# Optimization experiments

Hardware: AMD Instinct MI355X
Metric: run time of the kernel (lower is better)

## Reference

```python
import jax, jax.numpy as jnp
import numpy as np

EMB = 1024
HEADS = 16
HEAD_DIM = EMB // HEADS


def setup_inputs() -> dict:
    key = jax.random.key(0)
    ks = jax.random.split(key, 6)
    B, S = 4, 1024
    inputs = jax.random.normal(ks[0], (B, S, EMB), dtype=jnp.float32)
    # causal mask: 1.0 where attention is disallowed (added * -1e9 in the layer)
    mask = (1.0 - jnp.tril(jnp.ones((S, S), dtype=jnp.float32)))[None, None, :, :]
    scale = 1.0 / np.sqrt(EMB)
    wq = jax.random.normal(ks[1], (EMB, EMB), dtype=jnp.float32) * scale
    wk = jax.random.normal(ks[2], (EMB, EMB), dtype=jnp.float32) * scale
    wv = jax.random.normal(ks[3], (EMB, EMB), dtype=jnp.float32) * scale
    wo = jax.random.normal(ks[4], (EMB, EMB), dtype=jnp.float32) * scale
    zb = jnp.zeros((EMB,), dtype=jnp.float32)
    return {"inputs": inputs, "mask": mask, "wq": wq, "bq": zb, "wk": wk,
            "bk": zb, "wv": wv, "bv": zb, "wo": wo, "bo": zb}


def _split_heads(t, B):
    # [B, S, E] -> [B, H, S, Dh]
    return t.reshape(B, -1, HEADS, HEAD_DIM).transpose(0, 2, 1, 3)


def reference(inputs, mask, wq, bq, wk, bk, wv, bv, wo, bo):
    B = inputs.shape[0]
    q = _split_heads(inputs @ wq + bq, B)
    k = _split_heads(inputs @ wk + bk, B)
    v = _split_heads(inputs @ wv + bv, B)
    # NOTE: source divides by sqrt(sqrt(head_num)) = head_num**0.25
    scores = jnp.einsum('bhsd,bhtd->bhst', q, k) / jnp.asarray(HEADS, inputs.dtype) ** 0.25
    if mask is not None:
        scores = scores + mask * -1e9
    attn = jax.nn.softmax(scores, axis=-1)
    z = jnp.einsum('bhst,bhtd->bhsd', attn, v)
    # Faithful to source: reshape [B,H,S,Dh] -> [B,S,E] WITHOUT transposing heads back
    z = z.reshape(B, -1, EMB)
    return z @ wo + bo
```

## Files before the change

### kernel.cpp

```cpp
#include <hip/hip_runtime.h>
#include <hip/hip_bf16.h>
#include <stdint.h>

typedef __attribute__((ext_vector_type(8))) short short8;
typedef __attribute__((ext_vector_type(4))) float float4v;

#define SEQ   1024
#define NQKV  3072

__device__ __forceinline__ float bf2f(ushort h) {
    union { uint u; float f; } c; c.u = ((uint)h) << 16; return c.f;
}
__device__ __forceinline__ ushort f2bf(float f) {
    union { uint u; float f; } c; c.f = f;
    uint u = c.u;
    return (ushort)((u + 0x7fffu + ((u >> 16) & 1u)) >> 16);
}
__device__ __forceinline__ void gl2lds16(const ushort* g, ushort* l) {
    __builtin_amdgcn_global_load_lds(
        (const __attribute__((address_space(1))) unsigned int*)(g),
        (__attribute__((address_space(3))) unsigned int*)(l),
        16, 0, 0);
}

__global__ __launch_bounds__(256) void prep_k(const void* __restrict__ X,
                                              const void* __restrict__ w0,
                                              const void* __restrict__ w1,
                                              const void* __restrict__ w2,
                                              const void* __restrict__ w3,
                                              const void* __restrict__ bq,
                                              const void* __restrict__ bk,
                                              const void* __restrict__ bv,
                                              const void* __restrict__ bo,
                                              ushort* __restrict__ xc,
                                              ushort* __restrict__ biasout,
                                              ushort* __restrict__ wtall,
                                              int* __restrict__ flag) {
    __shared__ int tot;
    __shared__ ushort tile[64][72];
    int t = threadIdx.x;
    if (t == 0) tot = 0;
    __syncthreads();
    uint wv = ((const uint*)X)[t];
    uint e = (wv >> 7) & 0xFFu;
    bool isbf = (e >= 100u && e <= 130u);
    unsigned long long m = __ballot(isbf);
    if ((t & 63) == 0) atomicAdd(&tot, __popcll(m));
    __syncthreads();
    bool isf = (tot <= 128);

    int bi = blockIdx.x;
    if (bi == 0 && t == 0) flag[0] = isf ? 1 : 0;

    if (bi < 4096) {
        if (!isf) return;
        int i = (bi * 256 + t) * 4;
        float4 v = *(const float4*)((const float*)X + i);
        ushort4 o;
        o.x = f2bf(v.x); o.y = f2bf(v.y); o.z = f2bf(v.z); o.w = f2bf(v.w);
        *(ushort4*)(xc + i) = o;
    } else if (bi < 4112) {
        int i = (bi - 4096) * 256 + t;
        int sel = i >> 10, j = i & 1023;
        const void* p = (sel == 0) ? bq : (sel == 1) ? bk : (sel == 2) ? bv : bo;
        biasout[i] = isf ? f2bf(((const float*)p)[j]) : ((const ushort*)p)[j];
    } else {
        int idx = bi - 4112;
        int z = idx >> 8, rem = idx & 255;
        const void* in = (z == 0) ? w0 : (z == 1) ? w1 : (z == 2) ? w2 : w3;
        ushort* out = wtall + (size_t)z * 1024 * 1024;
        int k0 = (rem & 15) * 64, n0 = (rem >> 4) * 64;
        int r = t >> 3, c = (t & 7) * 8;
#pragma unroll
        for (int p = 0; p < 2; p++) {
            int rr = r + p * 32;
            if (isf) {
                const float* src = (const float*)in + (size_t)(k0 + rr) * 1024 + n0 + c;
                float4 v0 = *(const float4*)src;
                float4 v1 = *(const float4*)(src + 4);
                tile[rr][c + 0] = f2bf(v0.x); tile[rr][c + 1] = f2bf(v0.y);
                tile[rr][c + 2] = f2bf(v0.z); tile[rr][c + 3] = f2bf(v0.w);
                tile[rr][c + 4] = f2bf(v1.x); tile[rr][c + 5] = f2bf(v1.y);
                tile[rr][c + 6] = f2bf(v1.z); tile[rr][c + 7] = f2bf(v1.w);
            } else {
                uint4 v = *(const uint4*)((const ushort*)in + (size_t)(k0 + rr) * 1024 + n0 + c);
                *(uint4*)&tile[rr][c] = v;
            }
        }
        __syncthreads();
#pragma unroll
        for (int p = 0; p < 2; p++) {
            int n = r + p * 32;
            ushort vals[8];
#pragma unroll
            for (int j = 0; j < 8; j++) vals[j] = tile[c + j][n];
            *(uint4*)(out + (size_t)(n0 + n) * 1024 + k0 + c) = *(uint4*)vals;
        }
    }
}

__global__ __launch_bounds__(256) void vtrans_k(const ushort* __restrict__ qkv,
                                                ushort* __restrict__ vt) {
    __shared__ ushort tile[64][72];
    int t0 = blockIdx.x * 64;
    int bh = blockIdx.y;
    int b = bh >> 4, h = bh & 15;
    int t = threadIdx.x;
    int r = t >> 3, c = (t & 7) * 8;
#pragma unroll
    for (int p = 0; p < 2; p++) {
        int rr = r + p * 32;
        uint4 v = *(const uint4*)(qkv + (size_t)(b * 1024 + t0 + rr) * NQKV + 2048 + h * 64 + c);
        *(uint4*)&tile[rr][c] = v;
    }
    __syncthreads();
#pragma unroll
    for (int p = 0; p < 2; p++) {
        int d = r + p * 32;
        ushort vals[8];
#pragma unroll
        for (int j = 0; j < 8; j++) vals[j] = tile[c + j][d];
        *(uint4*)(vt + ((size_t)bh * 64 + d) * 1024 + t0 + c) = *(uint4*)vals;
    }
}

template <int BM, bool DUAL>
__global__ __launch_bounds__(256) void gemm_k(const ushort* __restrict__ Araw,
                                              const ushort* __restrict__ Aconv,
                                              const ushort* __restrict__ BT,
                                              const ushort* __restrict__ bias,
                                              void* __restrict__ C,
                                              const int* __restrict__ flag,
                                              int M, int N, int K) {
    constexpr int RM = BM / 32;
    __shared__ ushort As[BM * 64];
    __shared__ ushort Bs[128 * 64];
    int n0 = blockIdx.x * 128, m0 = blockIdx.y * BM;
    int t = threadIdx.x;
    int w = t >> 6, lane = t & 63, q = lane >> 4, ln = lane & 15;
    int wr = w >> 1, wc = w & 1;
    const ushort* A = (*flag) ? Aconv : Araw;

    float4v acc[RM][4];
#pragma unroll
    for (int r = 0; r < RM; r++)
#pragma unroll
        for (int cc = 0; cc < 4; cc++) acc[r][cc] = (float4v){0.f, 0.f, 0.f, 0.f};

    for (int k0 = 0; k0 < K; k0 += 64) {
#pragma unroll
        for (int j = 0; j < RM; j++) {
            int c = j * 256 + t;
            int row = c >> 3, s = c & 7;
            int kc = s ^ (row & 7);
            gl2lds16(A + (size_t)(m0 + row) * K + k0 + kc * 8, &As[c * 8]);
        }
#pragma unroll
        for (int j = 0; j < 4; j++) {
            int c = j * 256 + t;
            int row = c >> 3, s = c & 7;
            int kc = s ^ (row & 7);
            gl2lds16(BT + (size_t)(n0 + row) * K + k0 + kc * 8, &Bs[c * 8]);
        }
        __syncthreads();
#pragma unroll
        for (int half = 0; half < 2; half++) {
            int qc = half * 4 + q;
            short8 af[RM], bf[4];
#pragma unroll
            for (int r = 0; r < RM; r++) {
                int row = wr * (BM / 2) + r * 16 + ln;
                af[r] = *(const short8*)&As[((row << 3) | (qc ^ (row & 7))) * 8];
            }
#pragma unroll
            for (int cc = 0; cc < 4; cc++) {
                int col = wc * 64 + cc * 16 + ln;
                bf[cc] = *(const short8*)&Bs[((col << 3) | (qc ^ (col & 7))) * 8];
            }
#pragma unroll
            for (int r = 0; r < RM; r++)
#pragma unroll
                for (int cc = 0; cc < 4; cc++)
                    acc[r][cc] = __builtin_amdgcn_mfma_f32_16x16x32_bf16(af[r], bf[cc], acc[r][cc], 0, 0, 0);
        }
        __syncthreads();
    }

    bool outf = DUAL && (*flag != 0);
#pragma unroll
    for (int cc = 0; cc < 4; cc++) {
        int n = n0 + wc * 64 + cc * 16 + ln;
        float bs = bf2f(bias[n]);
#pragma unroll
        for (int r = 0; r < RM; r++) {
#pragma unroll
            for (int i = 0; i < 4; i++) {
                int m = m0 + wr * (BM / 2) + r * 16 + q * 4 + i;
                float v = acc[r][cc][i] + bs;
                if (outf) ((float*)C)[(size_t)m * N + n] = v;
                else      ((ushort*)C)[(size_t)m * N + n] = f2bf(v);
            }
        }
    }
}

__global__ __launch_bounds__(512) void attn_k(const ushort* __restrict__ qkv,
                                              const ushort* __restrict__ vt,
                                              ushort* __restrict__ zp) {
    __shared__ ushort Ks[2][64 * 64];
    __shared__ ushort Vs[2][64 * 64];
    __shared__ ushort P[8][16 * 76];
    int pr = blockIdx.x;
    int bh = blockIdx.y;
    int b = bh >> 4, h = bh & 15;
    int t = threadIdx.x;
    int w = t >> 6;
    int grp = w >> 2;
    int lane = t & 63, q = lane >> 4, ln = lane & 15;

    const float CE = 0.72134752f;

    const ushort* Qp = qkv + (size_t)(b * SEQ) * NQKV + h * 64;
    const ushort* Kp = qkv + (size_t)(b * SEQ) * NQKV + 1024 + h * 64;
    const ushort* Vt = vt + (size_t)bh * 64 * 1024;

    int row0 = t >> 3, kc0 = (t & 7) ^ (row0 & 7);

    int tiB = 15 - pr;
    int ti = grp ? tiB : pr;
    int sw = ti * 64 + (w & 3) * 16;

    short8 aq0 = *(const short8*)(Qp + (size_t)(sw + ln) * NQKV + q * 8);
    short8 aq1 = *(const short8*)(Qp + (size_t)(sw + ln) * NQKV + 32 + q * 8);

    float lp[4];
    float4v o[4];
#pragma unroll
    for (int i = 0; i < 4; i++) lp[i] = 0.f;
#pragma unroll
    for (int nb = 0; nb < 4; nb++) o[nb] = (float4v){0.f, 0.f, 0.f, 0.f};

    gl2lds16(Kp + (size_t)row0 * NQKV + kc0 * 8, &Ks[0][t * 8]);
    gl2lds16(Vt + (size_t)row0 * 1024 + kc0 * 8, &Vs[0][t * 8]);

    for (int kt = 0; kt <= tiB; kt++) {
        int cur = kt & 1;
        int t0 = kt * 64;
        __syncthreads();
        if (kt < tiB) {
            int nt0 = t0 + 64, nxt = cur ^ 1;
            gl2lds16(Kp + (size_t)(nt0 + row0) * NQKV + kc0 * 8, &Ks[nxt][t * 8]);
            gl2lds16(Vt + (size_t)row0 * 1024 + nt0 + kc0 * 8, &Vs[nxt][t * 8]);
        }
        if (kt <= ti) {
            float4v s[4];
#pragma unroll
            for (int nb = 0; nb < 4; nb++) {
                int row = nb * 16 + ln;
                short8 kf0 = *(const short8*)&Ks[cur][((row << 3) | (q ^ (row & 7))) * 8];
                short8 kf1 = *(const short8*)&Ks[cur][((row << 3) | ((4 + q) ^ (row & 7))) * 8];
                s[nb] = (float4v){0.f, 0.f, 0.f, 0.f};
                s[nb] = __builtin_amdgcn_mfma_f32_16x16x32_bf16(aq0, kf0, s[nb], 0, 0, 0);
                s[nb] = __builtin_amdgcn_mfma_f32_16x16x32_bf16(aq1, kf1, s[nb], 0, 0, 0);
            }
            float p[4][4];
            if (kt < ti) {
#pragma unroll
                for (int nb = 0; nb < 4; nb++)
#pragma unroll
                    for (int i = 0; i < 4; i++) p[nb][i] = exp2f(s[nb][i] * CE);
            } else {
#pragma unroll
                for (int nb = 0; nb < 4; nb++)
#pragma unroll
                    for (int i = 0; i < 4; i++) {
                        int srow = sw + q * 4 + i;
                        int col = t0 + nb * 16 + ln;
                        p[nb][i] = exp2f((col <= srow) ? s[nb][i] * CE : -1e30f);
                    }
            }
#pragma unroll
            for (int i = 0; i < 4; i++)
                lp[i] += (p[0][i] + p[1][i]) + (p[2][i] + p[3][i]);
#pragma unroll
            for (int nb = 0; nb < 4; nb++)
#pragma unroll
                for (int i = 0; i < 4; i++)
                    P[w][(q * 4 + i) * 76 + nb * 16 + ln] = f2bf(p[nb][i]);
            asm volatile("s_waitcnt lgkmcnt(0)\n" ::: "memory");
            short8 ap0 = *(const short8*)&P[w][ln * 76 + q * 8];
            short8 ap1 = *(const short8*)&P[w][ln * 76 + 32 + q * 8];
#pragma unroll
            for (int nb = 0; nb < 4; nb++) {
                int row = nb * 16 + ln;
                short8 bv0 = *(const short8*)&Vs[cur][((row << 3) | (q ^ (row & 7))) * 8];
                short8 bv1 = *(const short8*)&Vs[cur][((row << 3) | ((4 + q) ^ (row & 7))) * 8];
                o[nb] = __builtin_amdgcn_mfma_f32_16x16x32_bf16(ap0, bv0, o[nb], 0, 0, 0);
                o[nb] = __builtin_amdgcn_mfma_f32_16x16x32_bf16(ap1, bv1, o[nb], 0, 0, 0);
            }
        }
    }

    float l_i[4];
#pragma unroll
    for (int i = 0; i < 4; i++) {
        float s = lp[i];
#pragma unroll
        for (int mk = 1; mk < 16; mk <<= 1) s += __shfl_xor(s, mk, 64);
        l_i[i] = s;
    }
#pragma unroll
    for (int nb = 0; nb < 4; nb++) {
#pragma unroll
        for (int i = 0; i < 4; i++) {
            int srow = sw + q * 4 + i;
            int d = nb * 16 + ln;
            float z = o[nb][i] / l_i[i];
            int sp = h * 64 + (srow >> 4);
            int ep = ((srow & 15) << 6) + d;
            zp[((size_t)(b * SEQ + sp)) * 1024 + ep] = f2bf(z);
        }
    }
}

extern "C" void kernel_launch(void* const* d_in, const int* in_sizes, int n_in,
                              void* d_out, int out_size, void* d_ws, size_t ws_size,
                              hipStream_t stream) {
    const void* X  = d_in[0];
    const void* wq = d_in[2];
    const void* bq = d_in[3];
    const void* wk = d_in[4];
    const void* bk = d_in[5];
    const void* wv = d_in[6];
    const void* bv = d_in[7];
    const void* wo = d_in[8];
    const void* bo = d_in[9];

    char* ws = (char*)d_ws;
    int*    flag  = (int*)ws;
    ushort* biasq = (ushort*)(ws + 4096);
    ushort* WTall = (ushort*)(ws + 12288);
    ushort* Xc    = (ushort*)(ws + 8400896);
    ushort* QKV   = (ushort*)(ws + 16789504);
    ushort* VT    = (ushort*)(ws + 41955328);
    ushort* WTo   = WTall + 3 * 1024 * 1024;
    ushort* ZP    = Xc;

    prep_k<<<5136, 256, 0, stream>>>(X, wq, wk, wv, wo, bq, bk, bv, bo,
                                     Xc, biasq, WTall, flag);
    gemm_k<128, false><<<dim3(24, 32), 256, 0, stream>>>(
        (const ushort*)X, Xc, WTall, biasq, QKV, flag, 4096, NQKV, 1024);
    vtrans_k<<<dim3(16, 64), 256, 0, stream>>>(QKV, VT);
    attn_k<<<dim3(8, 64), 512, 0, stream>>>(QKV, VT, ZP);
    gemm_k<64, true><<<dim3(8, 64), 256, 0, stream>>>(
        ZP, ZP, WTo, biasq + 3072, d_out, flag, 4096, 1024, 1024);
}
```

Baseline: 196.9 us.

## Double-buffer GEMM LDS tiles with K-step 32 and prefetch next tile

The GEMM kernel now uses two LDS buffers of half the K depth (32 instead of 64), issuing global-to-LDS loads for the next K tile while MFMAs run on the current one. The swizzle changes to match the 4-chunk row layout, and one of the two barriers per iteration is dropped. This aims to hide global memory latency behind compute, at the cost of twice as many loop iterations with less MFMA work per barrier. There is also a possible hazard: the buffer being prefetched into was read by other waves in the previous iteration, and only the single barrier at the top orders those reads before the overwrite.

```diff
diff --git a/kernel.cpp b/kernel.cpp
--- a/kernel.cpp
+++ b/kernel.cpp
@@ -133,8 +133,9 @@
                                               const int* __restrict__ flag,
                                               int M, int N, int K) {
     constexpr int RM = BM / 32;
-    __shared__ ushort As[BM * 64];
-    __shared__ ushort Bs[128 * 64];
+    constexpr int AJ = BM / 64;
+    __shared__ ushort As[2][BM * 32];
+    __shared__ ushort Bs[2][128 * 32];
     int n0 = blockIdx.x * 128, m0 = blockIdx.y * BM;
     int t = threadIdx.x;
     int w = t >> 6, lane = t & 63, q = lane >> 4, ln = lane & 15;
@@ -147,43 +148,58 @@
 #pragma unroll
         for (int cc = 0; cc < 4; cc++) acc[r][cc] = (float4v){0.f, 0.f, 0.f, 0.f};
 
-    for (int k0 = 0; k0 < K; k0 += 64) {
-#pragma unroll
-        for (int j = 0; j < RM; j++) {
-            int c = j * 256 + t;
-            int row = c >> 3, s = c & 7;
-            int kc = s ^ (row & 7);
-            gl2lds16(A + (size_t)(m0 + row) * K + k0 + kc * 8, &As[c * 8]);
-        }
-#pragma unroll
-        for (int j = 0; j < 4; j++) {
-            int c = j * 256 + t;
-            int row = c >> 3, s = c & 7;
-            int kc = s ^ (row & 7);
-            gl2lds16(BT + (size_t)(n0 + row) * K + k0 + kc * 8, &Bs[c * 8]);
-        }
+#pragma unroll
+    for (int j = 0; j < AJ; j++) {
+        int c = j * 256 + t;
+        int row = c >> 2, s = c & 3;
+        int kc = s ^ ((row >> 1) & 3);
+        gl2lds16(A + (size_t)(m0 + row) * K + kc * 8, &As[0][c * 8]);
+    }
+#pragma unroll
+    for (int j = 0; j < 2; j++) {
+        int c = j * 256 + t;
+        int row = c >> 2, s = c & 3;
+        int kc = s ^ ((row >> 1) & 3);
+        gl2lds16(BT + (size_t)(n0 + row) * K + kc * 8, &Bs[0][c * 8]);
+    }
+
+    int nIter = K >> 5;
+    for (int kt = 0; kt < nIter; kt++) {
+        int cur = kt & 1;
         __syncthreads();
-#pragma unroll
-        for (int half = 0; half < 2; half++) {
-            int qc = half * 4 + q;
-            short8 af[RM], bf[4];
-#pragma unroll
-            for (int r = 0; r < RM; r++) {
-                int row = wr * (BM / 2) + r * 16 + ln;
-                af[r] = *(const short8*)&As[((row << 3) | (qc ^ (row & 7))) * 8];
-            }
-#pragma unroll
-            for (int cc = 0; cc < 4; cc++) {
-                int col = wc * 64 + cc * 16 + ln;
-                bf[cc] = *(const short8*)&Bs[((col << 3) | (qc ^ (col & 7))) * 8];
-            }
-#pragma unroll
-            for (int r = 0; r < RM; r++)
-#pragma unroll
-                for (int cc = 0; cc < 4; cc++)
-                    acc[r][cc] = __builtin_amdgcn_mfma_f32_16x16x32_bf16(af[r], bf[cc], acc[r][cc], 0, 0, 0);
-        }
-        __syncthreads();
+        if (kt + 1 < nIter) {
+            int nk0 = (kt + 1) << 5, nxt = cur ^ 1;
+#pragma unroll
+            for (int j = 0; j < AJ; j++) {
+                int c = j * 256 + t;
+                int row = c >> 2, s = c & 3;
+                int kc = s ^ ((row >> 1) & 3);
+                gl2lds16(A + (size_t)(m0 + row) * K + nk0 + kc * 8, &As[nxt][c * 8]);
+            }
+#pragma unroll
+            for (int j = 0; j < 2; j++) {
+                int c = j * 256 + t;
+                int row = c >> 2, s = c & 3;
+                int kc = s ^ ((row >> 1) & 3);
+                gl2lds16(BT + (size_t)(n0 + row) * K + nk0 + kc * 8, &Bs[nxt][c * 8]);
+            }
+        }
+        short8 af[RM], bf[4];
+#pragma unroll
+        for (int r = 0; r < RM; r++) {
+            int row = wr * (BM / 2) + r * 16 + ln;
+            af[r] = *(const short8*)&As[cur][((row << 2) | (q ^ ((row >> 1) & 3))) * 8];
+        }
+#pragma unroll
+        for (int cc = 0; cc < 4; cc++) {
+            int col = wc * 64 + cc * 16 + ln;
+            bf[cc] = *(const short8*)&Bs[cur][((col << 2) | (q ^ ((col >> 1) & 3))) * 8];
+        }
+#pragma unroll
+        for (int r = 0; r < RM; r++)
+#pragma unroll
+            for (int cc = 0; cc < 4; cc++)
+                acc[r][cc] = __builtin_amdgcn_mfma_f32_16x16x32_bf16(af[r], bf[cc], acc[r][cc], 0, 0, 0);
     }
 
     bool outf = DUAL && (*flag != 0);
```

After: 189.8 us. -3.6%, faster.
